# Performance work log

Measured on AMD Instinct MI355X. Metric: run time of the kernel, lower is better.

Reference implementation:

```python
import jax, jax.numpy as jnp
import numpy as np

T, B, V, D, H, C = 2048, 32, 50257, 512, 768, 10


def setup_inputs() -> dict:
    key = jax.random.key(0)
    ks = jax.random.split(key, 11)
    s = 0.02
    return {
        "x": jax.random.randint(ks[0], (T, B), 0, V),
        "embed_table": jax.random.normal(ks[1], (V, D), jnp.float32) * s,
        "W_x": jax.random.normal(ks[2], (H, D), jnp.float32) * s,
        "W_f": jax.random.normal(ks[3], (H, D), jnp.float32) * s,
        "b_f": jax.random.normal(ks[4], (H,), jnp.float32) * s,
        "W_r": jax.random.normal(ks[5], (H, D), jnp.float32) * s,
        "b_r": jax.random.normal(ks[6], (H,), jnp.float32) * s,
        "W_cx": jax.random.normal(ks[7], (H, D), jnp.float32) * s,
        "b_cx": jax.random.normal(ks[8], (H,), jnp.float32) * s,
        "W_out": jax.random.normal(ks[9], (C, H), jnp.float32) * s,
        "b_out": jax.random.normal(ks[10], (C,), jnp.float32) * s,
    }


def reference(x, embed_table, W_x, W_f, b_f, W_r, b_r, W_cx, b_cx, W_out, b_out):
    # Embedding lookup: [T, B, D]
    e = embed_table[x]
    # Precompute all gate projections for every timestep (batched GEMMs).
    xp = jnp.einsum("tbd,hd->tbh", e, W_x)                 # x_t projection
    f = jax.nn.sigmoid(jnp.einsum("tbd,hd->tbh", e, W_f) + b_f)   # forget gate
    r = jax.nn.sigmoid(jnp.einsum("tbd,hd->tbh", e, W_r) + b_r)   # reset gate
    cx = jnp.einsum("tbd,hd->tbh", e, W_cx) + b_cx                # highway path

    c0 = jnp.zeros((B, H), e.dtype)  # init_hidden: zeros

    def step(c, inp):
        f_t, xp_t, r_t, cx_t = inp
        c = f_t * c + (1.0 - f_t) * xp_t
        h = r_t * jnp.tanh(c) + (1.0 - r_t) * cx_t
        return c, h

    _, ht = jax.lax.scan(step, c0, (f, xp, r, cx))  # ht: [T, B, H]

    # tanh -> max-pool over time -> tanh -> classifier
    pooled = jnp.max(jnp.tanh(ht), axis=0)          # [B, H]
    pooled = jnp.tanh(pooled)
    logit = pooled @ W_out.T + b_out                # [B, C]
    return logit
```

## Files before the change

### kernel.cpp

```cpp
#include <hip/hip_runtime.h>
#include <hip/hip_bf16.h>
#include <cstdint>
#include <cstddef>

#define T_DIM 2048
#define B_DIM 32
#define D_DIM 512
#define H_DIM 768
#define C_DIM 10
#define K_DIM D_DIM
#define N_DIM (4 * H_DIM)

#define TC 1024
#define NCHUNK (T_DIM / TC)
#define MC (TC * B_DIM)

#define L_SEG 32
#define S_SEG (TC / L_SEG)
#define BH (B_DIM * H_DIM)

typedef __attribute__((ext_vector_type(8))) short short8;
typedef __attribute__((ext_vector_type(4))) float float4v;

__device__ inline unsigned short f2bf(float f) {
  unsigned int u = __builtin_bit_cast(unsigned int, f);
  unsigned int r = (u + 0x7FFFu + ((u >> 16) & 1u)) >> 16;
  return (unsigned short)r;
}
__device__ inline float bf2f(unsigned short s) {
  unsigned int u = ((unsigned int)s) << 16;
  return __builtin_bit_cast(float, u);
}
__device__ inline float fast_rcp(float x) { return __builtin_amdgcn_rcpf(x); }
__device__ inline float fast_exp2(float x) { return __builtin_amdgcn_exp2f(x); }
__device__ inline float sigmoid_f(float x) {
  float e = fast_exp2(-1.4426950408889634f * x);
  return fast_rcp(1.0f + e);
}
__device__ inline float tanh_f(float x) {
  float e = fast_exp2(2.885390081777927f * x);
  return 1.0f - 2.0f * fast_rcp(e + 1.0f);
}
__device__ inline void gld16(const unsigned short* g, unsigned short* l) {
  __builtin_amdgcn_global_load_lds(
      (const __attribute__((address_space(1))) void*)g,
      (__attribute__((address_space(3))) void*)l, 16, 0, 0);
}
__device__ inline unsigned int pack_bf16x2(float lo, float hi) {
  return ((unsigned int)f2bf(hi) << 16) | (unsigned int)f2bf(lo);
}

__global__ __launch_bounds__(256) void gather_embed_kernel(
    const int* __restrict__ x_c, const float* __restrict__ table,
    unsigned short* __restrict__ ebfc) {
  int idx = blockIdx.x * 256 + threadIdx.x;
  int m = idx >> 7;
  int k4 = (idx & 127) << 2;
  int row = x_c[m];
  float4 v = *(const float4*)(table + (size_t)row * D_DIM + k4);
  ushort4 o;
  o.x = f2bf(v.x); o.y = f2bf(v.y); o.z = f2bf(v.z); o.w = f2bf(v.w);
  *(ushort4*)(ebfc + (size_t)m * D_DIM + k4) = o;
}

__global__ __launch_bounds__(256) void convert_w_kernel(
    const float* __restrict__ Wx, const float* __restrict__ Wf,
    const float* __restrict__ Wr, const float* __restrict__ Wcx,
    unsigned short* __restrict__ wcat) {
  int idx = blockIdx.x * 256 + threadIdx.x;
  int n = idx >> 7;
  int k4 = (idx & 127) << 2;
  int mat = n / H_DIM;
  int h = n - mat * H_DIM;
  const float* src = (mat == 0) ? Wx : (mat == 1) ? Wf : (mat == 2) ? Wr : Wcx;
  float4 v = *(const float4*)(src + (size_t)h * D_DIM + k4);
  ushort4 o;
  o.x = f2bf(v.x); o.y = f2bf(v.y); o.z = f2bf(v.z); o.w = f2bf(v.w);
  *(ushort4*)(wcat + (size_t)n * D_DIM + k4) = o;
}

#define BMT 128
#define BNT 256
#define BKT 32
#define NT (K_DIM / BKT)
#define BUF_SH 12288

__device__ __forceinline__ float4v mfma16(short8 a, short8 b, float4v c) {
  return __builtin_amdgcn_mfma_f32_16x16x32_bf16(a, b, c, 0, 0, 0);
}

__device__ __forceinline__ void stgA(const unsigned short* srcA, unsigned short* sm,
                                     int buf, int kt, int tid) {
  const unsigned short* s = srcA + kt * BKT;
  unsigned short* d = sm + buf * BUF_SH + tid * 8;
  gld16(s, d);
  gld16(s + (size_t)128 * K_DIM, d + 4096);
}
__device__ __forceinline__ void stgB(const unsigned short* srcB, unsigned short* sm,
                                     int buf, int kt, int tid) {
  gld16(srcB + kt * BKT, sm + buf * BUF_SH + 8192 + tid * 8);
}

template <int STG, int VMN>
__device__ __forceinline__ void tile_step(
    int u, unsigned short* sm, const unsigned short* srcA,
    const unsigned short* srcB, int tid, int aO, int bO,
    float4v (&acc)[4][4]) {
  unsigned short* c = sm + (u % 3) * BUF_SH;
  const int sbuf = (u + 2) % 3;
  short8 a[4], b[4];
#pragma unroll
  for (int f = 0; f < 4; f++) a[f] = *(const short8*)(c + aO + f * 512);
  b[0] = *(const short8*)(c + bO);
  b[1] = *(const short8*)(c + bO + 512);
  if constexpr (STG) stgA(srcA, sm, sbuf, u + 2, tid);
  __builtin_amdgcn_sched_barrier(0);
  __builtin_amdgcn_s_barrier();
  __builtin_amdgcn_s_setprio(1);
#pragma unroll
  for (int f = 0; f < 4; f++) {
    acc[f][0] = mfma16(a[f], b[0], acc[f][0]);
    acc[f][1] = mfma16(a[f], b[1], acc[f][1]);
  }
  __builtin_amdgcn_s_setprio(0);
  __builtin_amdgcn_sched_barrier(0);
  b[2] = *(const short8*)(c + bO + 1024);
  b[3] = *(const short8*)(c + bO + 1536);
  if constexpr (STG) stgB(srcB, sm, sbuf, u + 2, tid);
  __builtin_amdgcn_sched_barrier(0);
  __builtin_amdgcn_s_setprio(1);
#pragma unroll
  for (int f = 0; f < 4; f++) {
    acc[f][2] = mfma16(a[f], b[2], acc[f][2]);
    acc[f][3] = mfma16(a[f], b[3], acc[f][3]);
  }
  __builtin_amdgcn_s_setprio(0);
  __builtin_amdgcn_sched_barrier(0);
  if constexpr (VMN == 3)
    asm volatile("s_waitcnt vmcnt(3)" ::: "memory");
  else if constexpr (VMN == 0)
    asm volatile("s_waitcnt vmcnt(0)" ::: "memory");
  __builtin_amdgcn_s_barrier();
}

__global__ __launch_bounds__(512, 4) void gemm_kernel(
    const unsigned short* __restrict__ ebfc,
    const unsigned short* __restrict__ wcat,
    const float* __restrict__ b_f, const float* __restrict__ b_r,
    const float* __restrict__ b_cx,
    unsigned short* __restrict__ projc) {
  __shared__ __align__(16) unsigned short smem[36864];

  const int tid = threadIdx.x;
  const int wave = tid >> 6;
  const int lane = tid & 63;
  const int quad = lane >> 4;
  const int l16 = lane & 15;
  const int wn = wave >> 1;
  const int wm = wave & 1;

  const int orig = blockIdx.x;
  const int swz = (orig & 7) * 384 + (orig >> 3);
  const int n_idx = swz % 12;
  const int m_idx = swz / 12;
  const int n0 = n_idx * BNT;
  const int m0 = m_idx * BMT;

  const int arow = tid >> 2;
  const int kchx = (tid & 3) ^ ((arow >> 1) & 3);
  const unsigned short* srcA = wcat + (size_t)(n0 + arow) * K_DIM + kchx * 8;
  const unsigned short* srcB = ebfc + (size_t)(m0 + arow) * K_DIM + kchx * 8;

  const int xr = (quad ^ ((l16 >> 1) & 3)) * 8;
  const int aO = (wn * 64 + l16) * 32 + xr;
  const int bO = 8192 + (wm * 64 + l16) * 32 + xr;

  float4v acc[4][4] = {};

  stgA(srcA, smem, 0, 0, tid);
  stgB(srcB, smem, 0, 0, tid);
  stgA(srcA, smem, 1, 1, tid);
  stgB(srcB, smem, 1, 1, tid);
  asm volatile("s_waitcnt vmcnt(3)" ::: "memory");
  __builtin_amdgcn_s_barrier();

#pragma unroll
  for (int u = 0; u < NT - 2; u++)
    tile_step<1, 3>(u, smem, srcA, srcB, tid, aO, bO, acc);
  tile_step<0, 0>(NT - 2, smem, srcA, srcB, tid, aO, bO, acc);
  tile_step<0, -1>(NT - 1, smem, srcA, srcB, tid, aO, bO, acc);

  __syncthreads();
  int mat = n0 / H_DIM;
  int hb = n0 - mat * H_DIM;
  size_t matBase = (size_t)mat * MC * H_DIM;
  const float* bias = (mat == 1) ? b_f : (mat == 2) ? b_r : b_cx;
#pragma unroll
  for (int f = 0; f < 4; f++) {
    int hl = wn * 64 + f * 16 + quad * 4;
    float4 bv;
    if (mat == 0) { bv.x = bv.y = bv.z = bv.w = 0.0f; }
    else          { bv = *(const float4*)(bias + hb + hl); }
#pragma unroll
    for (int g = 0; g < 4; g++) {
      int ml = wm * 64 + g * 16 + l16;
      float v0 = acc[f][g][0] + bv.x;
      float v1 = acc[f][g][1] + bv.y;
      float v2 = acc[f][g][2] + bv.z;
      float v3 = acc[f][g][3] + bv.w;
      if (mat == 1 || mat == 2) {
        v0 = sigmoid_f(v0); v1 = sigmoid_f(v1);
        v2 = sigmoid_f(v2); v3 = sigmoid_f(v3);
      }
      uint2 pk;
      pk.x = pack_bf16x2(v0, v1);
      pk.y = pack_bf16x2(v2, v3);
      int log8 = hl >> 2;
      int phys8 = log8 ^ ((ml & 7) << 1);
      *(uint2*)(smem + ml * 256 + phys8 * 4) = pk;
    }
  }
  __syncthreads();
#pragma unroll
  for (int it = 0; it < 8; it++) {
    int idx = it * 512 + tid;
    int ml = idx >> 5;
    int c16 = idx & 31;
    int phys16 = c16 ^ (ml & 7);
    short8 v = *(const short8*)(smem + ml * 256 + phys16 * 8);
    *(short8*)(projc + matBase + (size_t)(m0 + ml) * H_DIM + hb + c16 * 8) = v;
  }
}

__global__ __launch_bounds__(128) void scan1_kernel(
    const unsigned short* __restrict__ projc,
    float* __restrict__ Pw, float* __restrict__ Qw) {
  int blk = blockIdx.x;
  int seg = blk / (BH / 512);
  int q   = blk % (BH / 512);
  int e4  = (q * 128 + threadIdx.x) * 4;
  const size_t mstr = (size_t)MC * H_DIM;
  size_t idx0 = (size_t)(seg * L_SEG) * BH + e4;
  float p0 = 1.f, p1 = 1.f, p2 = 1.f, p3 = 1.f;
  float c0 = 0.f, c1 = 0.f, c2 = 0.f, c3 = 0.f;
#pragma unroll 4
  for (int t = 0; t < L_SEG; t++) {
    size_t id = idx0 + (size_t)t * BH;
    ushort4 xp = *(const ushort4*)(projc + id);
    ushort4 ff = *(const ushort4*)(projc + mstr + id);
    float f0 = bf2f(ff.x), f1 = bf2f(ff.y), f2 = bf2f(ff.z), f3 = bf2f(ff.w);
    c0 = fmaf(f0, c0 - bf2f(xp.x), bf2f(xp.x));
    c1 = fmaf(f1, c1 - bf2f(xp.y), bf2f(xp.y));
    c2 = fmaf(f2, c2 - bf2f(xp.z), bf2f(xp.z));
    c3 = fmaf(f3, c3 - bf2f(xp.w), bf2f(xp.w));
    p0 *= f0; p1 *= f1; p2 *= f2; p3 *= f3;
  }
  int o = seg * BH + e4;
  *(float4*)(Pw + o) = make_float4(p0, p1, p2, p3);
  *(float4*)(Qw + o) = make_float4(c0, c1, c2, c3);
}

__global__ __launch_bounds__(256) void prefix_kernel(
    const float* __restrict__ Pw, const float* __restrict__ Qw,
    float* __restrict__ cin, float* __restrict__ c_state,
    const float* __restrict__ segmax, float* __restrict__ hm_state,
    int first, int hm_init) {
  int gid = blockIdx.x * 256 + threadIdx.x;
  float c = first ? 0.f : c_state[gid];
#pragma unroll
  for (int s = 0; s < S_SEG; s++) {
    cin[s * BH + gid] = c;
    c = fmaf(Pw[s * BH + gid], c, Qw[s * BH + gid]);
  }
  c_state[gid] = c;
  if (!first) {
    float m = segmax[gid];
#pragma unroll
    for (int s = 1; s < S_SEG; s++) m = fmaxf(m, segmax[s * BH + gid]);
    hm_state[gid] = hm_init ? m : fmaxf(hm_state[gid], m);
  }
}

__global__ __launch_bounds__(128) void scan2_kernel(
    const unsigned short* __restrict__ projc,
    const float* __restrict__ cin, float* __restrict__ segmax) {
  int blk = blockIdx.x;
  int seg = blk / (BH / 512);
  int q   = blk % (BH / 512);
  int e4  = (q * 128 + threadIdx.x) * 4;
  const size_t mstr = (size_t)MC * H_DIM;
  size_t idx0 = (size_t)(seg * L_SEG) * BH + e4;
  int o = seg * BH + e4;
  float4 cv = *(const float4*)(cin + o);
  float c0 = cv.x, c1 = cv.y, c2 = cv.z, c3 = cv.w;
  float m0 = -1e30f, m1 = -1e30f, m2 = -1e30f, m3 = -1e30f;
#pragma unroll 2
  for (int t = 0; t < L_SEG; t++) {
    size_t id = idx0 + (size_t)t * BH;
    ushort4 xp = *(const ushort4*)(projc + id);
    ushort4 ff = *(const ushort4*)(projc + mstr + id);
    ushort4 rr = *(const ushort4*)(projc + 2 * mstr + id);
    ushort4 cx = *(const ushort4*)(projc + 3 * mstr + id);
    c0 = fmaf(bf2f(ff.x), c0 - bf2f(xp.x), bf2f(xp.x));
    c1 = fmaf(bf2f(ff.y), c1 - bf2f(xp.y), bf2f(xp.y));
    c2 = fmaf(bf2f(ff.z), c2 - bf2f(xp.z), bf2f(xp.z));
    c3 = fmaf(bf2f(ff.w), c3 - bf2f(xp.w), bf2f(xp.w));
    float h0 = fmaf(bf2f(rr.x), tanh_f(c0) - bf2f(cx.x), bf2f(cx.x));
    float h1 = fmaf(bf2f(rr.y), tanh_f(c1) - bf2f(cx.y), bf2f(cx.y));
    float h2 = fmaf(bf2f(rr.z), tanh_f(c2) - bf2f(cx.z), bf2f(cx.z));
    float h3 = fmaf(bf2f(rr.w), tanh_f(c3) - bf2f(cx.w), bf2f(cx.w));
    m0 = fmaxf(m0, h0); m1 = fmaxf(m1, h1);
    m2 = fmaxf(m2, h2); m3 = fmaxf(m3, h3);
  }
  *(float4*)(segmax + o) = make_float4(m0, m1, m2, m3);
}

__global__ __launch_bounds__(256) void pool_final_kernel(
    const float* __restrict__ segmax, const float* __restrict__ hm_state,
    float* __restrict__ pooled) {
  int gid = blockIdx.x * 256 + threadIdx.x;
  float m = hm_state[gid];
#pragma unroll
  for (int s = 0; s < S_SEG; s++) m = fmaxf(m, segmax[s * BH + gid]);
  pooled[gid] = tanh_f(tanh_f(m));
}

__global__ __launch_bounds__(64) void classifier_kernel(
    const float* __restrict__ pooled, const float* __restrict__ W_out,
    const float* __restrict__ b_out, float* __restrict__ out) {
  int b = blockIdx.x / C_DIM;
  int c = blockIdx.x % C_DIM;
  int lane = threadIdx.x;
  float s = 0.0f;
#pragma unroll
  for (int i = 0; i < H_DIM / 64; i++) {
    int h = i * 64 + lane;
    s += pooled[(size_t)b * H_DIM + h] * W_out[(size_t)c * H_DIM + h];
  }
#pragma unroll
  for (int off = 32; off; off >>= 1) s += __shfl_down(s, off, 64);
  if (lane == 0) out[b * C_DIM + c] = s + b_out[c];
}

extern "C" void kernel_launch(void* const* d_in, const int* in_sizes, int n_in,
                              void* d_out, int out_size, void* d_ws, size_t ws_size,
                              hipStream_t stream) {
  const int*   x     = (const int*)d_in[0];
  const float* table = (const float*)d_in[1];
  const float* W_x   = (const float*)d_in[2];
  const float* W_f   = (const float*)d_in[3];
  const float* b_f   = (const float*)d_in[4];
  const float* W_r   = (const float*)d_in[5];
  const float* b_r   = (const float*)d_in[6];
  const float* W_cx  = (const float*)d_in[7];
  const float* b_cx  = (const float*)d_in[8];
  const float* W_out = (const float*)d_in[9];
  const float* b_out = (const float*)d_in[10];

  char* ws = (char*)d_ws;
  size_t off = 0;
  unsigned short* wcat  = (unsigned short*)(ws + off); off += (size_t)N_DIM * K_DIM * 2;
  unsigned short* ebfc  = (unsigned short*)(ws + off); off += (size_t)MC * K_DIM * 2;
  unsigned short* projc = (unsigned short*)(ws + off); off += (size_t)4 * MC * H_DIM * 2;
  float* Pw     = (float*)(ws + off); off += (size_t)S_SEG * BH * 4;
  float* Qw     = (float*)(ws + off); off += (size_t)S_SEG * BH * 4;
  float* cin    = (float*)(ws + off); off += (size_t)S_SEG * BH * 4;
  float* segmax = (float*)(ws + off); off += (size_t)S_SEG * BH * 4;
  float* c_st   = (float*)(ws + off); off += (size_t)BH * 4;
  float* hm_st  = (float*)(ws + off); off += (size_t)BH * 4;
  float* pooled = (float*)(ws + off); off += (size_t)BH * 4;

  convert_w_kernel<<<(N_DIM * K_DIM / 4) / 256, 256, 0, stream>>>(W_x, W_f, W_r, W_cx, wcat);

  for (int ch = 0; ch < NCHUNK; ch++) {
    gather_embed_kernel<<<(MC * K_DIM / 4) / 256, 256, 0, stream>>>(x + (size_t)ch * MC, table, ebfc);
    gemm_kernel<<<(N_DIM / BNT) * (MC / BMT), 512, 0, stream>>>(ebfc, wcat, b_f, b_r, b_cx, projc);
    scan1_kernel<<<S_SEG * (BH / 512), 128, 0, stream>>>(projc, Pw, Qw);
    prefix_kernel<<<BH / 256, 256, 0, stream>>>(Pw, Qw, cin, c_st, segmax, hm_st,
                                                ch == 0, ch == 1);
    scan2_kernel<<<S_SEG * (BH / 512), 128, 0, stream>>>(projc, cin, segmax);
  }
  pool_final_kernel<<<BH / 256, 256, 0, stream>>>(segmax, hm_st, pooled);
  classifier_kernel<<<B_DIM * C_DIM, 64, 0, stream>>>(pooled, W_out, b_out, (float*)d_out);
}
```

Before: 523.4 us.

## Fuse segmented scan passes into one kernel with decoupled lookback chaining

```diff
diff --git a/kernel.cpp b/kernel.cpp
--- a/kernel.cpp
+++ b/kernel.cpp
@@ -18,6 +18,7 @@
 #define L_SEG 32
 #define S_SEG (TC / L_SEG)
 #define BH (B_DIM * H_DIM)
+#define NQ (BH / 512)
 
 typedef __attribute__((ext_vector_type(8))) short short8;
 typedef __attribute__((ext_vector_type(4))) float float4v;
@@ -52,7 +53,11 @@
 
 __global__ __launch_bounds__(256) void gather_embed_kernel(
     const int* __restrict__ x_c, const float* __restrict__ table,
-    unsigned short* __restrict__ ebfc) {
+    unsigned short* __restrict__ ebfc, int* __restrict__ flags) {
+  if (blockIdx.x == 0) {
+#pragma unroll
+    for (int i = threadIdx.x; i < S_SEG * NQ; i += 256) flags[i] = 0;
+  }
   int idx = blockIdx.x * 256 + threadIdx.x;
   int m = idx >> 7;
   int k4 = (idx & 127) << 2;
@@ -232,67 +237,75 @@
   }
 }
 
-__global__ __launch_bounds__(128) void scan1_kernel(
+__global__ __launch_bounds__(128) void scan_fused_kernel(
     const unsigned short* __restrict__ projc,
-    float* __restrict__ Pw, float* __restrict__ Qw) {
-  int blk = blockIdx.x;
-  int seg = blk / (BH / 512);
-  int q   = blk % (BH / 512);
-  int e4  = (q * 128 + threadIdx.x) * 4;
+    float* __restrict__ c_chain,
+    int* __restrict__ flags,
+    float* __restrict__ c_state,
+    float* __restrict__ segmax,
+    int first) {
+  const int blk = blockIdx.x;
+  const int seg = blk / NQ;
+  const int q = blk % NQ;
+  const int tid = threadIdx.x;
+  const int e4 = (q * 128 + tid) * 4;
   const size_t mstr = (size_t)MC * H_DIM;
-  size_t idx0 = (size_t)(seg * L_SEG) * BH + e4;
+  const size_t idx0 = (size_t)(seg * L_SEG) * BH + e4;
+
   float p0 = 1.f, p1 = 1.f, p2 = 1.f, p3 = 1.f;
-  float c0 = 0.f, c1 = 0.f, c2 = 0.f, c3 = 0.f;
+  float q0 = 0.f, q1 = 0.f, q2 = 0.f, q3 = 0.f;
 #pragma unroll 4
   for (int t = 0; t < L_SEG; t++) {
     size_t id = idx0 + (size_t)t * BH;
     ushort4 xp = *(const ushort4*)(projc + id);
     ushort4 ff = *(const ushort4*)(projc + mstr + id);
     float f0 = bf2f(ff.x), f1 = bf2f(ff.y), f2 = bf2f(ff.z), f3 = bf2f(ff.w);
-    c0 = fmaf(f0, c0 - bf2f(xp.x), bf2f(xp.x));
-    c1 = fmaf(f1, c1 - bf2f(xp.y), bf2f(xp.y));
-    c2 = fmaf(f2, c2 - bf2f(xp.z), bf2f(xp.z));
-    c3 = fmaf(f3, c3 - bf2f(xp.w), bf2f(xp.w));
+    q0 = fmaf(f0, q0 - bf2f(xp.x), bf2f(xp.x));
+    q1 = fmaf(f1, q1 - bf2f(xp.y), bf2f(xp.y));
+    q2 = fmaf(f2, q2 - bf2f(xp.z), bf2f(xp.z));
+    q3 = fmaf(f3, q3 - bf2f(xp.w), bf2f(xp.w));
     p0 *= f0; p1 *= f1; p2 *= f2; p3 *= f3;
   }
-  int o = seg * BH + e4;
-  *(float4*)(Pw + o) = make_float4(p0, p1, p2, p3);
-  *(float4*)(Qw + o) = make_float4(c0, c1, c2, c3);
-}
-
-__global__ __launch_bounds__(256) void prefix_kernel(
-    const float* __restrict__ Pw, const float* __restrict__ Qw,
-    float* __restrict__ cin, float* __restrict__ c_state,
-    const float* __restrict__ segmax, float* __restrict__ hm_state,
-    int first, int hm_init) {
-  int gid = blockIdx.x * 256 + threadIdx.x;
-  float c = first ? 0.f : c_state[gid];
-#pragma unroll
-  for (int s = 0; s < S_SEG; s++) {
-    cin[s * BH + gid] = c;
-    c = fmaf(Pw[s * BH + gid], c, Qw[s * BH + gid]);
-  }
-  c_state[gid] = c;
-  if (!first) {
-    float m = segmax[gid];
-#pragma unroll
-    for (int s = 1; s < S_SEG; s++) m = fmaxf(m, segmax[s * BH + gid]);
-    hm_state[gid] = hm_init ? m : fmaxf(hm_state[gid], m);
-  }
-}
-
-__global__ __launch_bounds__(128) void scan2_kernel(
-    const unsigned short* __restrict__ projc,
-    const float* __restrict__ cin, float* __restrict__ segmax) {
-  int blk = blockIdx.x;
-  int seg = blk / (BH / 512);
-  int q   = blk % (BH / 512);
-  int e4  = (q * 128 + threadIdx.x) * 4;
-  const size_t mstr = (size_t)MC * H_DIM;
-  size_t idx0 = (size_t)(seg * L_SEG) * BH + e4;
-  int o = seg * BH + e4;
-  float4 cv = *(const float4*)(cin + o);
-  float c0 = cv.x, c1 = cv.y, c2 = cv.z, c3 = cv.w;
+
+  float ci0, ci1, ci2, ci3;
+  if (seg == 0) {
+    if (first) {
+      ci0 = ci1 = ci2 = ci3 = 0.f;
+    } else {
+      float4 cv = *(const float4*)(c_state + e4);
+      ci0 = cv.x; ci1 = cv.y; ci2 = cv.z; ci3 = cv.w;
+    }
+  } else {
+    if (tid == 0) {
+      while (__hip_atomic_load(&flags[(seg - 1) * NQ + q], __ATOMIC_ACQUIRE,
+                               __HIP_MEMORY_SCOPE_AGENT) == 0)
+        __builtin_amdgcn_s_sleep(8);
+    }
+    __syncthreads();
+    const float* src = c_chain + (size_t)(seg - 1) * BH + e4;
+    ci0 = __hip_atomic_load(src + 0, __ATOMIC_RELAXED, __HIP_MEMORY_SCOPE_AGENT);
+    ci1 = __hip_atomic_load(src + 1, __ATOMIC_RELAXED, __HIP_MEMORY_SCOPE_AGENT);
+    ci2 = __hip_atomic_load(src + 2, __ATOMIC_RELAXED, __HIP_MEMORY_SCOPE_AGENT);
+    ci3 = __hip_atomic_load(src + 3, __ATOMIC_RELAXED, __HIP_MEMORY_SCOPE_AGENT);
+  }
+
+  float co0 = fmaf(p0, ci0, q0), co1 = fmaf(p1, ci1, q1);
+  float co2 = fmaf(p2, ci2, q2), co3 = fmaf(p3, ci3, q3);
+  {
+    float* dst = c_chain + (size_t)seg * BH + e4;
+    __hip_atomic_store(dst + 0, co0, __ATOMIC_RELAXED, __HIP_MEMORY_SCOPE_AGENT);
+    __hip_atomic_store(dst + 1, co1, __ATOMIC_RELAXED, __HIP_MEMORY_SCOPE_AGENT);
+    __hip_atomic_store(dst + 2, co2, __ATOMIC_RELAXED, __HIP_MEMORY_SCOPE_AGENT);
+    __hip_atomic_store(dst + 3, co3, __ATOMIC_RELAXED, __HIP_MEMORY_SCOPE_AGENT);
+  }
+  __syncthreads();
+  if (tid == 0)
+    __hip_atomic_store(&flags[seg * NQ + q], 1, __ATOMIC_RELEASE,
+                       __HIP_MEMORY_SCOPE_AGENT);
+  if (seg == S_SEG - 1)
+    *(float4*)(c_state + e4) = make_float4(co0, co1, co2, co3);
+
+  float c0 = ci0, c1 = ci1, c2 = ci2, c3 = ci3;
   float m0 = -1e30f, m1 = -1e30f, m2 = -1e30f, m3 = -1e30f;
 #pragma unroll 2
   for (int t = 0; t < L_SEG; t++) {
@@ -312,16 +325,16 @@
     m0 = fmaxf(m0, h0); m1 = fmaxf(m1, h1);
     m2 = fmaxf(m2, h2); m3 = fmaxf(m3, h3);
   }
-  *(float4*)(segmax + o) = make_float4(m0, m1, m2, m3);
+  *(float4*)(segmax + (size_t)seg * BH + e4) = make_float4(m0, m1, m2, m3);
 }
 
 __global__ __launch_bounds__(256) void pool_final_kernel(
-    const float* __restrict__ segmax, const float* __restrict__ hm_state,
-    float* __restrict__ pooled) {
+    const float* __restrict__ segmax2, float* __restrict__ pooled) {
   int gid = blockIdx.x * 256 + threadIdx.x;
-  float m = hm_state[gid];
-#pragma unroll
-  for (int s = 0; s < S_SEG; s++) m = fmaxf(m, segmax[s * BH + gid]);
+  float m = -1e30f;
+#pragma unroll
+  for (int s = 0; s < NCHUNK * S_SEG; s++)
+    m = fmaxf(m, segmax2[(size_t)s * BH + gid]);
   pooled[gid] = tanh_f(tanh_f(m));
 }
 
@@ -362,24 +375,21 @@
   unsigned short* wcat  = (unsigned short*)(ws + off); off += (size_t)N_DIM * K_DIM * 2;
   unsigned short* ebfc  = (unsigned short*)(ws + off); off += (size_t)MC * K_DIM * 2;
   unsigned short* projc = (unsigned short*)(ws + off); off += (size_t)4 * MC * H_DIM * 2;
-  float* Pw     = (float*)(ws + off); off += (size_t)S_SEG * BH * 4;
-  float* Qw     = (float*)(ws + off); off += (size_t)S_SEG * BH * 4;
-  float* cin    = (float*)(ws + off); off += (size_t)S_SEG * BH * 4;
-  float* segmax = (float*)(ws + off); off += (size_t)S_SEG * BH * 4;
-  float* c_st   = (float*)(ws + off); off += (size_t)BH * 4;
-  float* hm_st  = (float*)(ws + off); off += (size_t)BH * 4;
-  float* pooled = (float*)(ws + off); off += (size_t)BH * 4;
+  float* c_chain = (float*)(ws + off); off += (size_t)S_SEG * BH * 4;
+  float* segmax2 = (float*)(ws + off); off += (size_t)NCHUNK * S_SEG * BH * 4;
+  float* c_st    = (float*)(ws + off); off += (size_t)BH * 4;
+  float* pooled  = (float*)(ws + off); off += (size_t)BH * 4;
+  int*   flags   = (int*)(ws + off);   off += (size_t)S_SEG * NQ * 4;
 
   convert_w_kernel<<<(N_DIM * K_DIM / 4) / 256, 256, 0, stream>>>(W_x, W_f, W_r, W_cx, wcat);
 
   for (int ch = 0; ch < NCHUNK; ch++) {
-    gather_embed_kernel<<<(MC * K_DIM / 4) / 256, 256, 0, stream>>>(x + (size_t)ch * MC, table, ebfc);
+    gather_embed_kernel<<<(MC * K_DIM / 4) / 256, 256, 0, stream>>>(
+        x + (size_t)ch * MC, table, ebfc, flags);
     gemm_kernel<<<(N_DIM / BNT) * (MC / BMT), 512, 0, stream>>>(ebfc, wcat, b_f, b_r, b_cx, projc);
-    scan1_kernel<<<S_SEG * (BH / 512), 128, 0, stream>>>(projc, Pw, Qw);
-    prefix_kernel<<<BH / 256, 256, 0, stream>>>(Pw, Qw, cin, c_st, segmax, hm_st,
-                                                ch == 0, ch == 1);
-    scan2_kernel<<<S_SEG * (BH / 512), 128, 0, stream>>>(projc, cin, segmax);
-  }
-  pool_final_kernel<<<BH / 256, 256, 0, stream>>>(segmax, hm_st, pooled);
+    scan_fused_kernel<<<S_SEG * NQ, 128, 0, stream>>>(
+        projc, c_chain, flags, c_st, segmax2 + (size_t)ch * S_SEG * BH, ch == 0);
+  }
+  pool_final_kernel<<<BH / 256, 256, 0, stream>>>(segmax2, pooled);
   classifier_kernel<<<B_DIM * C_DIM, 64, 0, stream>>>(pooled, W_out, b_out, (float*)d_out);
 }
```

After: 1.671 ms. 219% more time.

## Fuse segment scan, prefix, and max-pool into a single block-local kernel

Applied to the files above, without the earlier changes.

```diff
diff --git a/kernel.cpp b/kernel.cpp
--- a/kernel.cpp
+++ b/kernel.cpp
@@ -232,66 +232,55 @@
   }
 }
 
-__global__ __launch_bounds__(128) void scan1_kernel(
+__global__ __launch_bounds__(512) void scan_fused_kernel(
     const unsigned short* __restrict__ projc,
-    float* __restrict__ Pw, float* __restrict__ Qw) {
-  int blk = blockIdx.x;
-  int seg = blk / (BH / 512);
-  int q   = blk % (BH / 512);
-  int e4  = (q * 128 + threadIdx.x) * 4;
+    float* __restrict__ c_state, float* __restrict__ hm,
+    float* __restrict__ pooled, int first) {
+  __shared__ float4 Pl[S_SEG][16];
+  __shared__ float4 Ql[S_SEG][16];
+  const int tid = threadIdx.x;
+  const int seg = tid >> 4;
+  const int slot = tid & 15;
+  const int q = blockIdx.x;
+  const int e4 = q * 64 + slot * 4;
   const size_t mstr = (size_t)MC * H_DIM;
-  size_t idx0 = (size_t)(seg * L_SEG) * BH + e4;
+  const size_t idx0 = (size_t)(seg * L_SEG) * BH + e4;
+
   float p0 = 1.f, p1 = 1.f, p2 = 1.f, p3 = 1.f;
-  float c0 = 0.f, c1 = 0.f, c2 = 0.f, c3 = 0.f;
+  float q0 = 0.f, q1 = 0.f, q2 = 0.f, q3 = 0.f;
 #pragma unroll 4
   for (int t = 0; t < L_SEG; t++) {
     size_t id = idx0 + (size_t)t * BH;
     ushort4 xp = *(const ushort4*)(projc + id);
     ushort4 ff = *(const ushort4*)(projc + mstr + id);
     float f0 = bf2f(ff.x), f1 = bf2f(ff.y), f2 = bf2f(ff.z), f3 = bf2f(ff.w);
-    c0 = fmaf(f0, c0 - bf2f(xp.x), bf2f(xp.x));
-    c1 = fmaf(f1, c1 - bf2f(xp.y), bf2f(xp.y));
-    c2 = fmaf(f2, c2 - bf2f(xp.z), bf2f(xp.z));
-    c3 = fmaf(f3, c3 - bf2f(xp.w), bf2f(xp.w));
+    q0 = fmaf(f0, q0 - bf2f(xp.x), bf2f(xp.x));
+    q1 = fmaf(f1, q1 - bf2f(xp.y), bf2f(xp.y));
+    q2 = fmaf(f2, q2 - bf2f(xp.z), bf2f(xp.z));
+    q3 = fmaf(f3, q3 - bf2f(xp.w), bf2f(xp.w));
     p0 *= f0; p1 *= f1; p2 *= f2; p3 *= f3;
   }
-  int o = seg * BH + e4;
-  *(float4*)(Pw + o) = make_float4(p0, p1, p2, p3);
-  *(float4*)(Qw + o) = make_float4(c0, c1, c2, c3);
-}
-
-__global__ __launch_bounds__(256) void prefix_kernel(
-    const float* __restrict__ Pw, const float* __restrict__ Qw,
-    float* __restrict__ cin, float* __restrict__ c_state,
-    const float* __restrict__ segmax, float* __restrict__ hm_state,
-    int first, int hm_init) {
-  int gid = blockIdx.x * 256 + threadIdx.x;
-  float c = first ? 0.f : c_state[gid];
-#pragma unroll
-  for (int s = 0; s < S_SEG; s++) {
-    cin[s * BH + gid] = c;
-    c = fmaf(Pw[s * BH + gid], c, Qw[s * BH + gid]);
-  }
-  c_state[gid] = c;
-  if (!first) {
-    float m = segmax[gid];
-#pragma unroll
-    for (int s = 1; s < S_SEG; s++) m = fmaxf(m, segmax[s * BH + gid]);
-    hm_state[gid] = hm_init ? m : fmaxf(hm_state[gid], m);
-  }
-}
-
-__global__ __launch_bounds__(128) void scan2_kernel(
-    const unsigned short* __restrict__ projc,
-    const float* __restrict__ cin, float* __restrict__ segmax) {
-  int blk = blockIdx.x;
-  int seg = blk / (BH / 512);
-  int q   = blk % (BH / 512);
-  int e4  = (q * 128 + threadIdx.x) * 4;
-  const size_t mstr = (size_t)MC * H_DIM;
-  size_t idx0 = (size_t)(seg * L_SEG) * BH + e4;
-  int o = seg * BH + e4;
-  float4 cv = *(const float4*)(cin + o);
+  Pl[seg][slot] = make_float4(p0, p1, p2, p3);
+  Ql[seg][slot] = make_float4(q0, q1, q2, q3);
+  __syncthreads();
+
+  if (tid < 64) {
+    int sl = tid >> 2, el = tid & 3;
+    int ge = q * 64 + sl * 4 + el;
+    float c = first ? 0.f : c_state[ge];
+#pragma unroll 4
+    for (int s = 0; s < S_SEG; s++) {
+      float* Pp = (float*)&Pl[s][sl];
+      const float* Qp = (const float*)&Ql[s][sl];
+      float P = Pp[el], Q = Qp[el];
+      Pp[el] = c;
+      c = fmaf(P, c, Q);
+    }
+    c_state[ge] = c;
+  }
+  __syncthreads();
+
+  float4 cv = Pl[seg][slot];
   float c0 = cv.x, c1 = cv.y, c2 = cv.z, c3 = cv.w;
   float m0 = -1e30f, m1 = -1e30f, m2 = -1e30f, m3 = -1e30f;
 #pragma unroll 2
@@ -312,17 +301,19 @@
     m0 = fmaxf(m0, h0); m1 = fmaxf(m1, h1);
     m2 = fmaxf(m2, h2); m3 = fmaxf(m3, h3);
   }
-  *(float4*)(segmax + o) = make_float4(m0, m1, m2, m3);
-}
-
-__global__ __launch_bounds__(256) void pool_final_kernel(
-    const float* __restrict__ segmax, const float* __restrict__ hm_state,
-    float* __restrict__ pooled) {
-  int gid = blockIdx.x * 256 + threadIdx.x;
-  float m = hm_state[gid];
-#pragma unroll
-  for (int s = 0; s < S_SEG; s++) m = fmaxf(m, segmax[s * BH + gid]);
-  pooled[gid] = tanh_f(tanh_f(m));
+  __syncthreads();
+  Ql[seg][slot] = make_float4(m0, m1, m2, m3);
+  __syncthreads();
+
+  if (tid < 64) {
+    int sl = tid >> 2, el = tid & 3;
+    int ge = q * 64 + sl * 4 + el;
+    float mm = -1e30f;
+#pragma unroll 4
+    for (int s = 0; s < S_SEG; s++) mm = fmaxf(mm, ((const float*)&Ql[s][sl])[el]);
+    if (first) hm[ge] = mm;
+    else       pooled[ge] = tanh_f(tanh_f(fmaxf(hm[ge], mm)));
+  }
 }
 
 __global__ __launch_bounds__(64) void classifier_kernel(
@@ -362,12 +353,8 @@
   unsigned short* wcat  = (unsigned short*)(ws + off); off += (size_t)N_DIM * K_DIM * 2;
   unsigned short* ebfc  = (unsigned short*)(ws + off); off += (size_t)MC * K_DIM * 2;
   unsigned short* projc = (unsigned short*)(ws + off); off += (size_t)4 * MC * H_DIM * 2;
-  float* Pw     = (float*)(ws + off); off += (size_t)S_SEG * BH * 4;
-  float* Qw     = (float*)(ws + off); off += (size_t)S_SEG * BH * 4;
-  float* cin    = (float*)(ws + off); off += (size_t)S_SEG * BH * 4;
-  float* segmax = (float*)(ws + off); off += (size_t)S_SEG * BH * 4;
   float* c_st   = (float*)(ws + off); off += (size_t)BH * 4;
-  float* hm_st  = (float*)(ws + off); off += (size_t)BH * 4;
+  float* hm     = (float*)(ws + off); off += (size_t)BH * 4;
   float* pooled = (float*)(ws + off); off += (size_t)BH * 4;
 
   convert_w_kernel<<<(N_DIM * K_DIM / 4) / 256, 256, 0, stream>>>(W_x, W_f, W_r, W_cx, wcat);
@@ -375,11 +362,7 @@
   for (int ch = 0; ch < NCHUNK; ch++) {
     gather_embed_kernel<<<(MC * K_DIM / 4) / 256, 256, 0, stream>>>(x + (size_t)ch * MC, table, ebfc);
     gemm_kernel<<<(N_DIM / BNT) * (MC / BMT), 512, 0, stream>>>(ebfc, wcat, b_f, b_r, b_cx, projc);
-    scan1_kernel<<<S_SEG * (BH / 512), 128, 0, stream>>>(projc, Pw, Qw);
-    prefix_kernel<<<BH / 256, 256, 0, stream>>>(Pw, Qw, cin, c_st, segmax, hm_st,
-                                                ch == 0, ch == 1);
-    scan2_kernel<<<S_SEG * (BH / 512), 128, 0, stream>>>(projc, cin, segmax);
-  }
-  pool_final_kernel<<<BH / 256, 256, 0, stream>>>(segmax, hm_st, pooled);
+    scan_fused_kernel<<<BH / 64, 512, 0, stream>>>(projc, c_st, hm, pooled, ch == 0);
+  }
   classifier_kernel<<<B_DIM * C_DIM, 64, 0, stream>>>(pooled, W_out, b_out, (float*)d_out);
 }
```

Result: no change. 525.6 us (+0.4%).
